# Optimization experiments

Hardware: AMD Instinct MI355X
Metric: run time of the kernel (lower is better)

## Reference

```python
import jax, jax.numpy as jnp
import numpy as np

N_NODES = 50000
N_EDGES = 800000
D_MODEL = 64
D_EDGE = 32
D_HIDDEN = 256
N_GRAPHS = 64
EPS = 1e-5


def setup_inputs() -> dict:
    key = jax.random.key(0)
    ks = jax.random.split(key, 16)
    h = jax.random.normal(ks[0], (N_NODES, D_MODEL), dtype=jnp.float32)
    edge_index = jax.random.randint(ks[1], (2, N_EDGES), 0, N_NODES, dtype=jnp.int64)
    edge_attr = jax.random.normal(ks[2], (N_EDGES, D_EDGE), dtype=jnp.float32)
    batch = jnp.sort(jax.random.randint(ks[3], (N_NODES,), 0, N_GRAPHS, dtype=jnp.int64))
    s_in = 1.0 / np.sqrt(2 * D_MODEL + D_EDGE)
    s_h = 1.0 / np.sqrt(D_HIDDEN)
    s_u = 1.0 / np.sqrt(2 * D_MODEL)
    return {
        "h": h,
        "edge_attr": edge_attr,
        "edge_index": edge_index,
        "batch": batch,
        "msg_w1": jax.random.normal(ks[4], (2 * D_MODEL + D_EDGE, D_HIDDEN), dtype=jnp.float32) * s_in,
        "msg_b1": jnp.zeros((D_HIDDEN,), dtype=jnp.float32),
        "msg_w2": jax.random.normal(ks[5], (D_HIDDEN, D_MODEL), dtype=jnp.float32) * s_h,
        "msg_b2": jnp.zeros((D_MODEL,), dtype=jnp.float32),
        "upd_w1": jax.random.normal(ks[6], (2 * D_MODEL, D_HIDDEN), dtype=jnp.float32) * s_u,
        "upd_b1": jnp.zeros((D_HIDDEN,), dtype=jnp.float32),
        "upd_w2": jax.random.normal(ks[7], (D_HIDDEN, D_MODEL), dtype=jnp.float32) * s_h,
        "upd_b2": jnp.zeros((D_MODEL,), dtype=jnp.float32),
        "gn_weight": jnp.ones((D_MODEL,), dtype=jnp.float32),
        "gn_bias": jnp.zeros((D_MODEL,), dtype=jnp.float32),
        "gn_alpha": jnp.ones((D_MODEL,), dtype=jnp.float32),
    }


def _graph_norm(h, batch, weight, bias, alpha):
    # GraphNorm: subtract alpha-scaled per-graph mean, divide by per-graph std.
    ones = jnp.ones((h.shape[0],), dtype=h.dtype)
    counts = jax.ops.segment_sum(ones, batch, num_segments=N_GRAPHS)
    counts = jnp.maximum(counts, 1.0)[:, None]  # [G, 1]
    mean = jax.ops.segment_sum(h, batch, num_segments=N_GRAPHS) / counts  # [G, d]
    h_c = h - alpha * mean[batch]  # [N, d]
    var = jax.ops.segment_sum(h_c * h_c, batch, num_segments=N_GRAPHS) / counts  # [G, d]
    return weight * h_c / jnp.sqrt(var[batch] + EPS) + bias


def reference(h, edge_attr, edge_index, batch,
              msg_w1, msg_b1, msg_w2, msg_b2,
              upd_w1, upd_b1, upd_w2, upd_b2,
              gn_weight, gn_bias, gn_alpha):
    src, dst = edge_index[0], edge_index[1]
    # m_ij = MLP([h_dst, h_src, e_ij])   (dropout inactive in eval mode)
    m_in = jnp.concatenate([h[dst], h[src], edge_attr], axis=-1)  # [E, 2d+de]
    m = jax.nn.silu(m_in @ msg_w1 + msg_b1) @ msg_w2 + msg_b2      # [E, d]
    # agg_i = sum over incoming edges
    agg = jax.ops.segment_sum(m, dst, num_segments=h.shape[0])     # [N, d]
    # h_i' = h_i + MLP([h_i, agg_i])
    upd_in = jnp.concatenate([h, agg], axis=-1)                    # [N, 2d]
    dh = jax.nn.silu(upd_in @ upd_w1 + upd_b1) @ upd_w2 + upd_b2   # [N, d]
    h = h + dh
    return _graph_norm(h, batch, gn_weight, gn_bias, gn_alpha)
```

## Files before the change

### kernel.cpp

```cpp
#include <hip/hip_runtime.h>
#include <hip/hip_bf16.h>
#include <stdint.h>

#define N_NODES   50000
#define N_EDGES   800000
#define D_MODEL   64
#define D_HIDDEN  256
#define N_GRAPHS  64
#define EPS_GN    1e-5f

#define NBINS_PAD 50176
#define NB_SCAN   196

typedef __attribute__((ext_vector_type(8))) short short8;
typedef __attribute__((ext_vector_type(4))) float f32x4;
typedef __attribute__((ext_vector_type(4))) float float4v;
typedef __attribute__((ext_vector_type(2))) unsigned int uint2v;
typedef __attribute__((ext_vector_type(4))) unsigned int uint4v;

static __device__ __forceinline__ short f2bf(float f) {
  union { float f; uint32_t u; } v; v.f = f;
  uint32_t r = (v.u + 0x7fffu + ((v.u >> 16) & 1u)) >> 16;
  return (short)(uint16_t)r;
}

static __device__ __forceinline__ uint32_t pack_bf16x2(float lo, float hi) {
  union { float f; uint32_t u; } a, b;
  a.f = lo; b.f = hi;
  uint32_t ra = a.u + 0x7fffu + ((a.u >> 16) & 1u);
  uint32_t rb = b.u + 0x7fffu + ((b.u >> 16) & 1u);
  return __builtin_amdgcn_perm(rb, ra, 0x07060302u);
}

static __device__ __forceinline__ float silu_f(float x) {
  return x * __builtin_amdgcn_rcpf(1.0f + __expf(-x));
}

static __device__ __forceinline__ f32x4 mfma16(short8 a, short8 b, f32x4 c) {
  return __builtin_amdgcn_mfma_f32_16x16x32_bf16(a, b, c, 0, 0, 0);
}

#define HBF_BLOCKS 1563

__global__ void prep_all(const float* __restrict__ mw1, const float* __restrict__ mw2,
                         const float* __restrict__ uw1, const float* __restrict__ uw2,
                         const float* __restrict__ h,
                         short* __restrict__ w1f, short* __restrict__ w2f,
                         short* __restrict__ u1f, short* __restrict__ u2f,
                         short* __restrict__ h_bf) {
  int b = blockIdx.x;
  if (b >= 52) {
    int t2 = (b - 52) * 256 + threadIdx.x;
    if (t2 < N_NODES * D_MODEL / 8) {
      const float4v* src = (const float4v*)(h + (size_t)t2 * 8);
      float4v v0 = src[0], v1 = src[1];
      uint4v p = {pack_bf16x2(v0.x, v0.y), pack_bf16x2(v0.z, v0.w),
                  pack_bf16x2(v1.x, v1.y), pack_bf16x2(v1.z, v1.w)};
      *(uint4v*)(h_bf + (size_t)t2 * 8) = p;
    }
    return;
  }
  const float* w; short* out; int K, Nn, t;
  if (b < 20)      { w = mw1; out = w1f; K = 160; Nn = 256; t = b * 256 + threadIdx.x; }
  else if (b < 28) { w = mw2; out = w2f; K = 256; Nn = 64;  t = (b - 20) * 256 + threadIdx.x; }
  else if (b < 44) { w = uw1; out = u1f; K = 128; Nn = 256; t = (b - 28) * 256 + threadIdx.x; }
  else             { w = uw2; out = u2f; K = 256; Nn = 64;  t = (b - 44) * 256 + threadIdx.x; }
  int total = (K >> 5) * (Nn >> 4) * 64;
  if (t >= total) return;
  int lane = t & 63;
  int rest = t >> 6;
  int ntN = Nn >> 4;
  int nt = rest % ntN;
  int kt = rest / ntN;
  int n  = nt * 16 + (lane & 15);
  int k0 = kt * 32 + (lane >> 4) * 8;
  short* o = out + (size_t)t * 8;
#pragma unroll
  for (int j = 0; j < 8; ++j)
    o[j] = f2bf(w[(size_t)(k0 + j) * Nn + n]);
}

__global__ __launch_bounds__(256)
void hist_k(const int* __restrict__ ei, int* __restrict__ hist) {
  int e = blockIdx.x * 256 + threadIdx.x;
  if (e >= N_EDGES) return;
  atomicAdd(&hist[ei[N_EDGES + e]], 1);
}

__global__ __launch_bounds__(256)
void scan1(const int* __restrict__ hist, int* __restrict__ offs,
           int* __restrict__ bsums) {
  __shared__ int tmp[256];
  int i = blockIdx.x * 256 + threadIdx.x;
  int v = hist[i];
  tmp[threadIdx.x] = v;
  __syncthreads();
#pragma unroll
  for (int d = 1; d < 256; d <<= 1) {
    int t = (threadIdx.x >= d) ? tmp[threadIdx.x - d] : 0;
    __syncthreads();
    tmp[threadIdx.x] += t;
    __syncthreads();
  }
  offs[i] = tmp[threadIdx.x] - v;
  if (threadIdx.x == 255) bsums[blockIdx.x] = tmp[255];
}

__global__ __launch_bounds__(256)
void scan2(const int* __restrict__ bsums, int* __restrict__ bpre) {
  __shared__ int tmp[256];
  int v = (threadIdx.x < NB_SCAN) ? bsums[threadIdx.x] : 0;
  tmp[threadIdx.x] = v;
  __syncthreads();
#pragma unroll
  for (int d = 1; d < 256; d <<= 1) {
    int t = (threadIdx.x >= d) ? tmp[threadIdx.x - d] : 0;
    __syncthreads();
    tmp[threadIdx.x] += t;
    __syncthreads();
  }
  bpre[threadIdx.x] = tmp[threadIdx.x] - v;
}

__global__ __launch_bounds__(256)
void scan3(int* __restrict__ offs, const int* __restrict__ bpre) {
  int i = blockIdx.x * 256 + threadIdx.x;
  offs[i] += bpre[blockIdx.x];
}

__global__ __launch_bounds__(256)
void scatter_k(const int* __restrict__ ei, int* __restrict__ offs,
               int* __restrict__ sorted) {
  int e = blockIdx.x * 256 + threadIdx.x;
  if (e >= N_EDGES) return;
  int d = ei[N_EDGES + e];
  int pos = atomicAdd(&offs[d], 1);
  sorted[pos] = e;
}

#define LDA_E 168
#define LDH   264
#define LDC   68

__global__ __launch_bounds__(256, 2)
void edge_mlp(const short* __restrict__ h_bf, const float* __restrict__ ea,
              const int* __restrict__ ei, const int* __restrict__ sorted,
              const short* __restrict__ w1f, const float* __restrict__ b1,
              const short* __restrict__ w2f, const float* __restrict__ b2,
              float* __restrict__ agg) {
  __shared__ __align__(16) short buf[64 * LDH];
  __shared__ __align__(16) float sC[64 * LDC];
  __shared__ int s_ids[4][48];

  const int tid  = threadIdx.x;
  const int lane = tid & 63;
  const int wave = tid >> 6;
  const int col  = lane & 15;
  const int quad = lane >> 4;
  const int eb   = blockIdx.x * 64 + wave * 16;
  short* sA = buf;
  short* sH = buf;

  if (lane < 48) {
    int i15 = lane & 15;
    int e0 = sorted[eb + i15];
    int v;
    if (lane < 16)      v = ei[e0];
    else if (lane < 32) v = ei[N_EDGES + e0];
    else                v = e0;
    s_ids[wave][lane] = v;
  }

#pragma unroll
  for (int it = 0; it < 2; ++it) {
    int idx = it * 64 + lane;
    int e = idx >> 3, c = idx & 7;
    int row = wave * 16 + e;
    int d = s_ids[wave][16 + e];
    int s = s_ids[wave][e];
    *(short8*)&sA[row * LDA_E + c * 8] =
        *(const short8*)(h_bf + (size_t)d * D_MODEL + c * 8);
    *(short8*)&sA[row * LDA_E + 64 + c * 8] =
        *(const short8*)(h_bf + (size_t)s * D_MODEL + c * 8);
  }
#pragma unroll
  for (int it = 0; it < 2; ++it) {
    int idx = it * 64 + lane;
    int e = idx >> 3, j = idx & 7;
    int row = wave * 16 + e;
    int eid = s_ids[wave][32 + e];
    float4v v = *(const float4v*)(ea + (size_t)eid * 32 + j * 4);
    uint2v p = {pack_bf16x2(v.x, v.y), pack_bf16x2(v.z, v.w)};
    *(uint2v*)&sA[row * LDA_E + 128 + j * 4] = p;
  }
  __syncthreads();

  f32x4 acc[4][4];
#pragma unroll
  for (int mt = 0; mt < 4; ++mt)
#pragma unroll
    for (int nt = 0; nt < 4; ++nt)
      acc[mt][nt] = (f32x4){0.f, 0.f, 0.f, 0.f};

  short8 bf[2][4];
#pragma unroll
  for (int nt = 0; nt < 4; ++nt)
    bf[0][nt] = *(const short8*)(w1f + (size_t)((wave * 4 + nt) * 64 + lane) * 8);

#pragma unroll
  for (int kt = 0; kt < 5; ++kt) {
    if (kt < 4) {
#pragma unroll
      for (int nt = 0; nt < 4; ++nt)
        bf[(kt + 1) & 1][nt] = *(const short8*)(
            w1f + (size_t)(((kt + 1) * 16 + wave * 4 + nt) * 64 + lane) * 8);
    }
    short8 af[4];
#pragma unroll
    for (int mt = 0; mt < 4; ++mt)
      af[mt] = *(const short8*)&sA[(mt * 16 + col) * LDA_E + kt * 32 + quad * 8];
#pragma unroll
    for (int nt = 0; nt < 4; ++nt)
#pragma unroll
      for (int mt = 0; mt < 4; ++mt)
        acc[mt][nt] = mfma16(af[mt], bf[kt & 1][nt], acc[mt][nt]);
  }
  __syncthreads();

#pragma unroll
  for (int nt = 0; nt < 4; ++nt) {
    const int n = (wave * 4 + nt) * 16 + col;
    const float bias = b1[n];
#pragma unroll
    for (int mt = 0; mt < 4; ++mt) {
#pragma unroll
      for (int r = 0; r < 4; ++r) {
        const int row = mt * 16 + quad * 4 + r;
        sH[row * LDH + n] = f2bf(silu_f(acc[mt][nt][r] + bias));
      }
    }
  }
  __syncthreads();

  f32x4 acc2[4];
#pragma unroll
  for (int mt = 0; mt < 4; ++mt) acc2[mt] = (f32x4){0.f, 0.f, 0.f, 0.f};

  short8 bf2[2];
  bf2[0] = *(const short8*)(w2f + (size_t)(wave * 64 + lane) * 8);

#pragma unroll
  for (int kt = 0; kt < 8; ++kt) {
    if (kt < 7)
      bf2[(kt + 1) & 1] = *(const short8*)(
          w2f + (size_t)(((kt + 1) * 4 + wave) * 64 + lane) * 8);
    short8 af[4];
#pragma unroll
    for (int mt = 0; mt < 4; ++mt)
      af[mt] = *(const short8*)&sH[(mt * 16 + col) * LDH + kt * 32 + quad * 8];
#pragma unroll
    for (int mt = 0; mt < 4; ++mt)
      acc2[mt] = mfma16(af[mt], bf2[kt & 1], acc2[mt]);
  }

  {
    const int n = wave * 16 + col;
    const float bias = b2[n];
#pragma unroll
    for (int mt = 0; mt < 4; ++mt)
#pragma unroll
      for (int r = 0; r < 4; ++r)
        sC[(mt * 16 + quad * 4 + r) * LDC + n] = acc2[mt][r] + bias;
  }
  __syncthreads();

  float sum = 0.f;
  int prev = s_ids[wave][16];
#pragma unroll
  for (int r = 0; r < 16; ++r) {
    float v = sC[(wave * 16 + r) * LDC + lane];
    int d = s_ids[wave][16 + r];
    if (d != prev) {
      atomicAdd(agg + (size_t)prev * D_MODEL + lane, sum);
      sum = 0.f; prev = d;
    }
    sum += v;
  }
  atomicAdd(agg + (size_t)prev * D_MODEL + lane, sum);
}

#define LDA_N 136

__global__ __launch_bounds__(256, 2)
void node_mlp(const float* __restrict__ h, const short* __restrict__ h_bf,
              const float* __restrict__ agg,
              const short* __restrict__ w1f, const float* __restrict__ b1,
              const short* __restrict__ w2f, const float* __restrict__ b2,
              const int* __restrict__ batch,
              float* __restrict__ hnew,
              float* __restrict__ s1, float* __restrict__ s2,
              float* __restrict__ cnt) {
  __shared__ __align__(16) short buf[64 * LDH];
  __shared__ int s_b[64];

  const int tid  = threadIdx.x;
  const int lane = tid & 63;
  const int wave = tid >> 6;
  const int col  = lane & 15;
  const int quad = lane >> 4;
  const int nb   = blockIdx.x * 64;
  short* sA = buf;
  short* sH = buf;

  if (tid < 64) {
    int gi = nb + tid;
    s_b[tid] = batch[(gi < N_NODES) ? gi : (N_NODES - 1)];
  }

#pragma unroll
  for (int it = 0; it < 2; ++it) {
    int idx = it * 64 + lane;
    int i = idx >> 3, c = idx & 7;
    int row = wave * 16 + i;
    int gi = nb + row;
    if (gi >= N_NODES) gi = N_NODES - 1;
    *(short8*)&sA[row * LDA_N + c * 8] =
        *(const short8*)(h_bf + (size_t)gi * D_MODEL + c * 8);
  }
#pragma unroll
  for (int it = 0; it < 4; ++it) {
    int idx = it * 64 + lane;
    int i = idx >> 4, j = idx & 15;
    int row = wave * 16 + i;
    int gi = nb + row;
    if (gi >= N_NODES) gi = N_NODES - 1;
    float4v v = *(const float4v*)(agg + (size_t)gi * D_MODEL + j * 4);
    uint2v p = {pack_bf16x2(v.x, v.y), pack_bf16x2(v.z, v.w)};
    *(uint2v*)&sA[row * LDA_N + 64 + j * 4] = p;
  }
  __syncthreads();

  if (wave == 3) {
    int gi = nb + lane;
    bool valid = gi < N_NODES;
    int g = s_b[lane];
    int gp = __shfl_up(g, 1);
    bool start = valid && (lane == 0 || g != gp);
    unsigned long long bmask = __ballot(start);
    unsigned long long imask = __ballot(!valid);
    if (start) {
      unsigned long long higher =
          (lane == 63) ? 0ULL : (((bmask | imask) >> (lane + 1)) << (lane + 1));
      int next = higher ? (__ffsll((long long)higher) - 1) : 64;
      atomicAdd(&cnt[g], (float)(next - lane));
    }
  }

  f32x4 acc[4][4];
#pragma unroll
  for (int mt = 0; mt < 4; ++mt)
#pragma unroll
    for (int nt = 0; nt < 4; ++nt)
      acc[mt][nt] = (f32x4){0.f, 0.f, 0.f, 0.f};

  short8 bf[2][4];
#pragma unroll
  for (int nt = 0; nt < 4; ++nt)
    bf[0][nt] = *(const short8*)(w1f + (size_t)((wave * 4 + nt) * 64 + lane) * 8);

#pragma unroll
  for (int kt = 0; kt < 4; ++kt) {
    if (kt < 3) {
#pragma unroll
      for (int nt = 0; nt < 4; ++nt)
        bf[(kt + 1) & 1][nt] = *(const short8*)(
            w1f + (size_t)(((kt + 1) * 16 + wave * 4 + nt) * 64 + lane) * 8);
    }
    short8 af[4];
#pragma unroll
    for (int mt = 0; mt < 4; ++mt)
      af[mt] = *(const short8*)&sA[(mt * 16 + col) * LDA_N + kt * 32 + quad * 8];
#pragma unroll
    for (int nt = 0; nt < 4; ++nt)
#pragma unroll
      for (int mt = 0; mt < 4; ++mt)
        acc[mt][nt] = mfma16(af[mt], bf[kt & 1][nt], acc[mt][nt]);
  }
  __syncthreads();

#pragma unroll
  for (int nt = 0; nt < 4; ++nt) {
    const int n = (wave * 4 + nt) * 16 + col;
    const float bias = b1[n];
#pragma unroll
    for (int mt = 0; mt < 4; ++mt) {
#pragma unroll
      for (int r = 0; r < 4; ++r) {
        const int row = mt * 16 + quad * 4 + r;
        sH[row * LDH + n] = f2bf(silu_f(acc[mt][nt][r] + bias));
      }
    }
  }
  __syncthreads();

  f32x4 acc2[4];
#pragma unroll
  for (int mt = 0; mt < 4; ++mt) acc2[mt] = (f32x4){0.f, 0.f, 0.f, 0.f};

  short8 bf2[2];
  bf2[0] = *(const short8*)(w2f + (size_t)(wave * 64 + lane) * 8);

#pragma unroll
  for (int kt = 0; kt < 8; ++kt) {
    if (kt < 7)
      bf2[(kt + 1) & 1] = *(const short8*)(
          w2f + (size_t)(((kt + 1) * 4 + wave) * 64 + lane) * 8);
    short8 af[4];
#pragma unroll
    for (int mt = 0; mt < 4; ++mt)
      af[mt] = *(const short8*)&sH[(mt * 16 + col) * LDH + kt * 32 + quad * 8];
#pragma unroll
    for (int mt = 0; mt < 4; ++mt)
      acc2[mt] = mfma16(af[mt], bf2[kt & 1], acc2[mt]);
  }

  {
    const int n = wave * 16 + col;
    const float bias = b2[n];
    float a1 = 0.f, a2 = 0.f;
    int prev = s_b[quad * 4];
#pragma unroll
    for (int mt = 0; mt < 4; ++mt) {
#pragma unroll
      for (int r = 0; r < 4; ++r) {
        const int row = mt * 16 + quad * 4 + r;
        const int gi = nb + row;
        const bool valid = gi < N_NODES;
        int g = s_b[row];
        if (g != prev) {
          atomicAdd(&s1[prev * D_MODEL + n], a1);
          atomicAdd(&s2[prev * D_MODEL + n], a2);
          a1 = 0.f; a2 = 0.f; prev = g;
        }
        if (valid) {
          float hv = h[(size_t)gi * D_MODEL + n] + acc2[mt][r] + bias;
          hnew[(size_t)gi * D_MODEL + n] = hv;
          a1 += hv; a2 += hv * hv;
        }
      }
    }
    atomicAdd(&s1[prev * D_MODEL + n], a1);
    atomicAdd(&s2[prev * D_MODEL + n], a2);
  }
}

__global__ __launch_bounds__(256)
void gn_norm(float* __restrict__ x, const int* __restrict__ batch,
             const float* __restrict__ s1, const float* __restrict__ s2,
             const float* __restrict__ cnt, const float* __restrict__ alpha,
             const float* __restrict__ weight, const float* __restrict__ bias) {
  int idx = blockIdx.x * 256 + threadIdx.x;
  if (idx >= N_NODES * D_MODEL) return;
  int i = idx >> 6, f = idx & 63;
  int g = batch[i];
  float c = fmaxf(cnt[g], 1.f);
  float m   = s1[g * D_MODEL + f] / c;
  float ex2 = s2[g * D_MODEL + f] / c;
  float a = alpha[f];
  float var = ex2 - 2.f * a * m * m + a * a * m * m;
  float hc = x[idx] - a * m;
  x[idx] = weight[f] * hc * rsqrtf(var + EPS_GN) + bias[f];
}

extern "C" void kernel_launch(void* const* d_in, const int* in_sizes, int n_in,
                              void* d_out, int out_size, void* d_ws, size_t ws_size,
                              hipStream_t stream) {
  const float* h     = (const float*)d_in[0];
  const float* ea    = (const float*)d_in[1];
  const int*   ei    = (const int*)d_in[2];
  const int*   batch = (const int*)d_in[3];
  const float* mw1   = (const float*)d_in[4];
  const float* mb1   = (const float*)d_in[5];
  const float* mw2   = (const float*)d_in[6];
  const float* mb2   = (const float*)d_in[7];
  const float* uw1   = (const float*)d_in[8];
  const float* ub1   = (const float*)d_in[9];
  const float* uw2   = (const float*)d_in[10];
  const float* ub2   = (const float*)d_in[11];
  const float* gw    = (const float*)d_in[12];
  const float* gb    = (const float*)d_in[13];
  const float* ga    = (const float*)d_in[14];

  char* ws = (char*)d_ws;
  float* agg    = (float*)(ws + 0);
  short* w1f    = (short*)(ws + 12800000);
  short* w2f    = (short*)(ws + 12881920);
  short* u1f    = (short*)(ws + 12914688);
  short* u2f    = (short*)(ws + 12980224);
  float* s1     = (float*)(ws + 13012992);
  float* s2     = (float*)(ws + 13029376);
  float* cnt    = (float*)(ws + 13045760);
  int*   hist   = (int*)  (ws + 13046016);
  int*   offs   = (int*)  (ws + 13246720);
  int*   bsums  = (int*)  (ws + 13447424);
  int*   bpre   = (int*)  (ws + 13448448);
  int*   sorted = (int*)  (ws + 13449472);
  short* h_bf   = (short*)(ws + 16649472);

  hipMemsetAsync(agg, 0, 12800000, stream);
  hipMemsetAsync(ws + 13012992, 0, 33024, stream);
  hipMemsetAsync(hist, 0, 200704, stream);

  prep_all<<<52 + HBF_BLOCKS, 256, 0, stream>>>(mw1, mw2, uw1, uw2, h,
                                                w1f, w2f, u1f, u2f, h_bf);

  hist_k  <<<(N_EDGES + 255) / 256, 256, 0, stream>>>(ei, hist);
  scan1   <<<NB_SCAN, 256, 0, stream>>>(hist, offs, bsums);
  scan2   <<<1, 256, 0, stream>>>(bsums, bpre);
  scan3   <<<NB_SCAN, 256, 0, stream>>>(offs, bpre);
  scatter_k<<<(N_EDGES + 255) / 256, 256, 0, stream>>>(ei, offs, sorted);

  edge_mlp<<<N_EDGES / 64, 256, 0, stream>>>(h_bf, ea, ei, sorted,
                                             w1f, mb1, w2f, mb2, agg);

  node_mlp<<<(N_NODES + 63) / 64, 256, 0, stream>>>(h, h_bf, agg,
                                                    u1f, ub1, u2f, ub2,
                                                    batch, (float*)d_out,
                                                    s1, s2, cnt);

  gn_norm<<<(N_NODES * D_MODEL + 255) / 256, 256, 0, stream>>>(
      (float*)d_out, batch, s1, s2, cnt, ga, gw, gb);
}
```

Baseline: 458.1 us.

## Permute hidden layout for packed bf16 stores and aggregate edges from registers

```diff
diff --git a/kernel.cpp b/kernel.cpp
--- a/kernel.cpp
+++ b/kernel.cpp
@@ -30,6 +30,12 @@
   uint32_t ra = a.u + 0x7fffu + ((a.u >> 16) & 1u);
   uint32_t rb = b.u + 0x7fffu + ((b.u >> 16) & 1u);
   return __builtin_amdgcn_perm(rb, ra, 0x07060302u);
+}
+
+static __device__ __forceinline__ uint32_t cvt_pk_bf16(float lo, float hi) {
+  uint32_t r;
+  asm("v_cvt_pk_bf16_f32 %0, %1, %2" : "=v"(r) : "v"(lo), "v"(hi));
+  return r;
 }
 
 static __device__ __forceinline__ float silu_f(float x) {
@@ -67,6 +73,7 @@
   else             { w = uw2; out = u2f; K = 256; Nn = 64;  t = (b - 44) * 256 + threadIdx.x; }
   int total = (K >> 5) * (Nn >> 4) * 64;
   if (t >= total) return;
+  const bool permK = (K == 256);
   int lane = t & 63;
   int rest = t >> 6;
   int ntN = Nn >> 4;
@@ -76,8 +83,11 @@
   int k0 = kt * 32 + (lane >> 4) * 8;
   short* o = out + (size_t)t * 8;
 #pragma unroll
-  for (int j = 0; j < 8; ++j)
-    o[j] = f2bf(w[(size_t)(k0 + j) * Nn + n]);
+  for (int j = 0; j < 8; ++j) {
+    int kk = k0 + j;
+    int kr = permK ? ((kk >> 6) * 4 + (kk & 3)) * 16 + ((kk >> 2) & 15) : kk;
+    o[j] = f2bf(w[(size_t)kr * Nn + n]);
+  }
 }
 
 __global__ __launch_bounds__(256)
@@ -140,16 +150,14 @@
 
 #define LDA_E 168
 #define LDH   264
-#define LDC   68
-
-__global__ __launch_bounds__(256, 2)
+
+__global__ __launch_bounds__(256, 4)
 void edge_mlp(const short* __restrict__ h_bf, const float* __restrict__ ea,
               const int* __restrict__ ei, const int* __restrict__ sorted,
               const short* __restrict__ w1f, const float* __restrict__ b1,
               const short* __restrict__ w2f, const float* __restrict__ b2,
               float* __restrict__ agg) {
   __shared__ __align__(16) short buf[64 * LDH];
-  __shared__ __align__(16) float sC[64 * LDC];
   __shared__ int s_ids[4][48];
 
   const int tid  = threadIdx.x;
@@ -227,16 +235,21 @@
   }
   __syncthreads();
 
-#pragma unroll
-  for (int nt = 0; nt < 4; ++nt) {
-    const int n = (wave * 4 + nt) * 16 + col;
-    const float bias = b1[n];
+  {
+    float b1v[4];
+#pragma unroll
+    for (int nt = 0; nt < 4; ++nt) b1v[nt] = b1[(wave * 4 + nt) * 16 + col];
 #pragma unroll
     for (int mt = 0; mt < 4; ++mt) {
 #pragma unroll
       for (int r = 0; r < 4; ++r) {
         const int row = mt * 16 + quad * 4 + r;
-        sH[row * LDH + n] = f2bf(silu_f(acc[mt][nt][r] + bias));
+        float v0 = silu_f(acc[mt][0][r] + b1v[0]);
+        float v1 = silu_f(acc[mt][1][r] + b1v[1]);
+        float v2 = silu_f(acc[mt][2][r] + b1v[2]);
+        float v3 = silu_f(acc[mt][3][r] + b1v[3]);
+        uint2v p = {cvt_pk_bf16(v0, v1), cvt_pk_bf16(v2, v3)};
+        *(uint2v*)&sH[row * LDH + wave * 64 + col * 4] = p;
       }
     }
   }
@@ -266,32 +279,28 @@
   {
     const int n = wave * 16 + col;
     const float bias = b2[n];
-#pragma unroll
-    for (int mt = 0; mt < 4; ++mt)
-#pragma unroll
-      for (int r = 0; r < 4; ++r)
-        sC[(mt * 16 + quad * 4 + r) * LDC + n] = acc2[mt][r] + bias;
-  }
-  __syncthreads();
-
-  float sum = 0.f;
-  int prev = s_ids[wave][16];
-#pragma unroll
-  for (int r = 0; r < 16; ++r) {
-    float v = sC[(wave * 16 + r) * LDC + lane];
-    int d = s_ids[wave][16 + r];
-    if (d != prev) {
-      atomicAdd(agg + (size_t)prev * D_MODEL + lane, sum);
-      sum = 0.f; prev = d;
-    }
-    sum += v;
-  }
-  atomicAdd(agg + (size_t)prev * D_MODEL + lane, sum);
+    float sum = 0.f;
+    int prev = -1;
+#pragma unroll
+    for (int mt = 0; mt < 4; ++mt) {
+#pragma unroll
+      for (int r = 0; r < 4; ++r) {
+        const int row = mt * 16 + quad * 4 + r;
+        int d = s_ids[row >> 4][16 + (row & 15)];
+        if (d != prev) {
+          if (prev >= 0) atomicAdd(agg + (size_t)prev * D_MODEL + n, sum);
+          sum = 0.f; prev = d;
+        }
+        sum += acc2[mt][r] + bias;
+      }
+    }
+    atomicAdd(agg + (size_t)prev * D_MODEL + n, sum);
+  }
 }
 
 #define LDA_N 136
 
-__global__ __launch_bounds__(256, 2)
+__global__ __launch_bounds__(256, 4)
 void node_mlp(const float* __restrict__ h, const short* __restrict__ h_bf,
               const float* __restrict__ agg,
               const short* __restrict__ w1f, const float* __restrict__ b1,
@@ -388,16 +397,21 @@
   }
   __syncthreads();
 
-#pragma unroll
-  for (int nt = 0; nt < 4; ++nt) {
-    const int n = (wave * 4 + nt) * 16 + col;
-    const float bias = b1[n];
+  {
+    float b1v[4];
+#pragma unroll
+    for (int nt = 0; nt < 4; ++nt) b1v[nt] = b1[(wave * 4 + nt) * 16 + col];
 #pragma unroll
     for (int mt = 0; mt < 4; ++mt) {
 #pragma unroll
       for (int r = 0; r < 4; ++r) {
         const int row = mt * 16 + quad * 4 + r;
-        sH[row * LDH + n] = f2bf(silu_f(acc[mt][nt][r] + bias));
+        float v0 = silu_f(acc[mt][0][r] + b1v[0]);
+        float v1 = silu_f(acc[mt][1][r] + b1v[1]);
+        float v2 = silu_f(acc[mt][2][r] + b1v[2]);
+        float v3 = silu_f(acc[mt][3][r] + b1v[3]);
+        uint2v p = {cvt_pk_bf16(v0, v1), cvt_pk_bf16(v2, v3)};
+        *(uint2v*)&sH[row * LDH + wave * 64 + col * 4] = p;
       }
     }
   }
```

After: 502.0 us. 1.1x slower.
